# Performance work log

Hardware: AMD Instinct MI355X
Metric: run time of the kernel (lower is better)

Reference implementation:

```python
import jax, jax.numpy as jnp
import numpy as np
from jax import lax

B, S = 32, 256
V, D = 32000, 300   # pretrained word embeddings
P, PD = 35, 32      # pos vocab / pos embed dim (from source)
M = 66              # morph feature dim
H = 6               # LSTM units per direction -> bilstm_output_size = 12
A = 12


def _lstm(x, Wx, Wh, b, reverse=False):
    # x: [B,S,F] -> h: [B,S,H]; keras gate order i,f,c,o
    xg = x @ Wx + b  # precompute input projection once: [B,S,4H]
    def step(carry, xt):
        h, c = carry
        g = xt + h @ Wh
        i, f, cand, o = jnp.split(g, 4, axis=-1)
        c = jax.nn.sigmoid(f) * c + jax.nn.sigmoid(i) * jnp.tanh(cand)
        h = jax.nn.sigmoid(o) * jnp.tanh(c)
        return (h, c), h
    h0 = jnp.zeros((x.shape[0], Wh.shape[0]), x.dtype)
    _, hs = lax.scan(step, (h0, h0), jnp.swapaxes(xg, 0, 1), reverse=reverse)
    return jnp.swapaxes(hs, 0, 1)


def setup_inputs() -> dict:
    key = jax.random.key(0)
    ks = jax.random.split(key, 16)
    F = D + PD + M
    n = lambda k, shp, s=0.1: jax.random.normal(k, shp, dtype=jnp.float32) * s
    return {
        'words': jax.random.randint(ks[0], (B, S), 0, V),
        'pos': jax.random.randint(ks[1], (B, S), 0, P),
        'morph': jax.random.uniform(ks[2], (B, S, M), dtype=jnp.float32),
        'heads': jax.random.randint(ks[3], (B, S), 0, S),
        'word_table': n(ks[4], (V, D)),
        'pos_table': n(ks[5], (P, PD)),
        'Wx_f': n(ks[6], (F, 4 * H)), 'Wh_f': n(ks[7], (H, 4 * H)), 'b_f': jnp.zeros((4 * H,), jnp.float32),
        'Wx_b': n(ks[8], (F, 4 * H)), 'Wh_b': n(ks[9], (H, 4 * H)), 'b_b': jnp.zeros((4 * H,), jnp.float32),
        'Wu': n(ks[10], (A, A)), 'bu': jnp.zeros((A,), jnp.float32),
        'Ww': n(ks[11], (A, A)), 'bw': jnp.zeros((A,), jnp.float32),
        'v': n(ks[12], (A,)),
    }


def reference(words, pos, morph, heads, word_table, pos_table,
              Wx_f, Wh_f, b_f, Wx_b, Wh_b, b_b, Wu, bu, Ww, bw, v):
    # embed + concat -> [B,S,F]
    feats = jnp.concatenate([word_table[words], pos_table[pos], morph], axis=-1)
    # BiLSTM encoder -> [B,S,12] (dropout disabled / eval)
    hf = _lstm(feats, Wx_f, Wh_f, b_f)
    hb = _lstm(feats, Wx_b, Wh_b, b_b, reverse=True)
    repr_ = jnp.concatenate([hf, hb], axis=-1)
    # Bahdanau arc scoring, vectorized over dependant i (the tf loop):
    # scores[b,i,j] = v . tanh(u_a(repr)[b,j] + w_a(repr)[b,i])
    ua = repr_ @ Wu + bu  # head-position term (j)
    wa = repr_ @ Ww + bw  # dependant term (i)
    scores = jnp.einsum('bijd,d->bij', jnp.tanh(ua[:, None, :, :] + wa[:, :, None, :]), v)
    # the equality-based mask in tf picks out j == i (self cannot be head)
    eye = jnp.eye(S, dtype=bool)
    scores = jnp.where(eye[None], -10000.0, scores)
    # per-step sparse CE (from_logits, mean over batch), summed over i=1..S-1
    logp = jax.nn.log_softmax(scores, axis=-1)
    ce = -jnp.take_along_axis(logp, heads[:, :, None], axis=2)[..., 0]  # [B,S]
    loss = jnp.sum(jnp.mean(ce[:, 1:], axis=0))
    # parent_prob_table: exp(scores) concatenated along axis 0, i-major as in tf loop
    table = jnp.swapaxes(jnp.exp(scores[:, 1:, :]), 0, 1).reshape((S - 1) * B, S)
    return loss, table
```

## Files before the change

kernel.cpp:

```cpp
#include <hip/hip_runtime.h>
#include <hip/hip_bf16.h>

#define BB 32
#define SS 256
#define DD 300
#define PDD 32
#define MM 66
#define FF 398
#define HH 6
#define G4 24
#define AA 12
#define L2E 1.4426950408889634f

__device__ __forceinline__ float fast_rcp(float x) { return __builtin_amdgcn_rcpf(x); }
__device__ __forceinline__ float fast_tanh(float x) {
    return 1.f - 2.f * fast_rcp(__expf(2.f * x) + 1.f);
}
__device__ __forceinline__ float bcast_lane(float x, int l) {
    return __int_as_float(__builtin_amdgcn_readlane(__float_as_int(x), l));
}
template<int CTRL>
__device__ __forceinline__ float quad_bcast(float v) {
    return __int_as_float(__builtin_amdgcn_mov_dpp(__float_as_int(v), CTRL, 0xf, 0xf, true));
}

#define EPB 32
__global__ __launch_bounds__(256) void k_embed_proj(
    const int* __restrict__ words, const int* __restrict__ pos,
    const float* __restrict__ morph, const float* __restrict__ wtab,
    const float* __restrict__ ptab,
    const float* __restrict__ Wxf, const float* __restrict__ bfv,
    const float* __restrict__ Wxb, const float* __restrict__ bbv,
    float* __restrict__ xgf, float* __restrict__ xgb)
{
    __shared__ float4 sF[100][33];
    __shared__ float4 sW[48 * 100];
    int t  = threadIdx.x;
    int p0 = blockIdx.x * EPB;

    for (int idx = t; idx < EPB * 75; idx += 256) {
        int p = idx / 75, q = idx % 75;
        sF[q][p] = *(const float4*)(wtab + (size_t)words[p0 + p] * DD + 4 * q);
    }
    {
        int idx = t;
        int p = idx / 8, q = idx % 8;
        sF[75 + q][p] = *(const float4*)(ptab + pos[p0 + p] * PDD + 4 * q);
    }
    for (int idx = t; idx < EPB * 17; idx += 256) {
        int p = idx / 17, mq = idx % 17;
        const float2* ms = (const float2*)(morph + (size_t)(p0 + p) * MM);
        float2 lo = ms[2 * mq];
        float2 hi = (mq < 16) ? ms[2 * mq + 1] : make_float2(0.f, 0.f);
        sF[83 + mq][p] = make_float4(lo.x, lo.y, hi.x, hi.y);
    }
    {
        float* sWf = (float*)sW;
        for (int idx = t; idx < FF * G4; idx += 256) {
            int k = idx / G4, j = idx % G4;
            sWf[j * 400 + k]        = Wxf[idx];
            sWf[(24 + j) * 400 + k] = Wxb[idx];
        }
        if (t < 2 * G4) {
            int j = t >> 1, k = 398 + (t & 1);
            sWf[j * 400 + k] = 0.f; sWf[(24 + j) * 400 + k] = 0.f;
        }
    }
    __syncthreads();

    int lane = t & 63, w = t >> 6;
    int p    = lane & 31;
    int cg   = w * 2 + (lane >> 5);
    int dir  = cg >> 2;
    int tg   = cg & 3;
    int j0   = tg * 6;
    const float4* wc = sW + (dir * 24 + j0) * 100;

    float a0 = 0.f, a1 = 0.f, a2 = 0.f, a3 = 0.f, a4 = 0.f, a5 = 0.f;
    #pragma unroll 4
    for (int q = 0; q < 100; ++q) {
        float4 f = sF[q][p];
        float4 w0 = wc[0 * 100 + q], w1 = wc[1 * 100 + q], w2 = wc[2 * 100 + q];
        float4 w3 = wc[3 * 100 + q], w4 = wc[4 * 100 + q], w5 = wc[5 * 100 + q];
        a0 = fmaf(f.x, w0.x, a0); a0 = fmaf(f.y, w0.y, a0);
        a0 = fmaf(f.z, w0.z, a0); a0 = fmaf(f.w, w0.w, a0);
        a1 = fmaf(f.x, w1.x, a1); a1 = fmaf(f.y, w1.y, a1);
        a1 = fmaf(f.z, w1.z, a1); a1 = fmaf(f.w, w1.w, a1);
        a2 = fmaf(f.x, w2.x, a2); a2 = fmaf(f.y, w2.y, a2);
        a2 = fmaf(f.z, w2.z, a2); a2 = fmaf(f.w, w2.w, a2);
        a3 = fmaf(f.x, w3.x, a3); a3 = fmaf(f.y, w3.y, a3);
        a3 = fmaf(f.z, w3.z, a3); a3 = fmaf(f.w, w3.w, a3);
        a4 = fmaf(f.x, w4.x, a4); a4 = fmaf(f.y, w4.y, a4);
        a4 = fmaf(f.z, w4.z, a4); a4 = fmaf(f.w, w4.w, a4);
        a5 = fmaf(f.x, w5.x, a5); a5 = fmaf(f.y, w5.y, a5);
        a5 = fmaf(f.z, w5.z, a5); a5 = fmaf(f.w, w5.w, a5);
    }

    float kk = (tg == 2) ? 2.f * L2E : -L2E;
    const float* bias = dir ? bbv : bfv;
    float* o = (dir ? xgb : xgf) + (size_t)(p0 + p) * G4 + j0;
    o[0] = (a0 + bias[j0 + 0]) * kk; o[1] = (a1 + bias[j0 + 1]) * kk;
    o[2] = (a2 + bias[j0 + 2]) * kk; o[3] = (a3 + bias[j0 + 3]) * kk;
    o[4] = (a4 + bias[j0 + 4]) * kk; o[5] = (a5 + bias[j0 + 5]) * kk;
}

__global__ __launch_bounds__(64) void k_lstm(
    const float* __restrict__ xgf, const float* __restrict__ xgb,
    const float* __restrict__ Whf, const float* __restrict__ Whb,
    float* __restrict__ repr)
{
    __shared__ float sxg[(SS + 8) * G4];
    __shared__ float hbuf[SS * HH];
    int blk = blockIdx.x;
    int dir = blk >> 5;
    int b   = blk & 31;
    int lane = threadIdx.x;

    const float* xg = (dir ? xgb : xgf) + (size_t)b * SS * G4;
    const float* Wh = dir ? Whb : Whf;

    {
        const float4* src = (const float4*)xg;
        float4* dst = (float4*)sxg;
        #pragma unroll
        for (int u = 0; u < 24; ++u) {
            int d = lane + u * 64;
            int row = d / 6, c4 = d - row * 6;
            int drow = dir ? (SS - 1 - row) : row;
            dst[drow * 6 + c4] = src[d];
        }
        for (int g2 = lane; g2 < 8 * G4; g2 += 64) sxg[SS * G4 + g2] = 0.f;
    }

    int g    = lane % G4;
    int cell = g >> 2;
    int type = g & 3;
    int j    = type * HH + cell;

    float kk = (type == 2) ? 2.f * L2E : -L2E;
    float wh[HH];
    #pragma unroll
    for (int m = 0; m < HH; ++m) wh[m] = Wh[m * G4 + j] * kk;
    float Bc = (type == 2) ? 1.f : 0.f;
    float Ac = (type == 2) ? -1.f : 1.f;

    float sh[HH];
    #pragma unroll
    for (int m = 0; m < HH; ++m) sh[m] = 0.f;
    float c = 0.f;
    bool wr = (lane < G4) && ((lane & 3) == 0);
    __syncthreads();

    const float* xb = sxg + j;

    float pg[4];
    #pragma unroll
    for (int sl = 0; sl < 4; ++sl) pg[sl] = xb[sl * G4];

    #pragma unroll 1
    for (int t = 0; t < SS; t += 4) {
        #pragma unroll
        for (int sl = 0; sl < 4; ++sl) {
            float x = pg[sl];
            pg[sl] = xb[(t + 4 + sl) * G4];

            float aa  = fmaf(sh[1], wh[1], fmaf(sh[0], wh[0], x));
            float bb2 = fmaf(sh[3], wh[3], sh[2] * wh[2]);
            float cc2 = fmaf(sh[5], wh[5], sh[4] * wh[4]);
            x = (aa + bb2) + cc2;

            float e   = __builtin_amdgcn_exp2f(x);
            float val = fmaf(Bc, e, Ac) * fast_rcp(1.f + e);

            float vi = quad_bcast<0>(val);
            float vf = quad_bcast<85>(val);
            float vc = quad_bcast<170>(val);
            float vo = quad_bcast<255>(val);

            c = fmaf(vf, c, vi * vc);
            float ec = __builtin_amdgcn_exp2f(c * (2.f * L2E));
            float h  = (ec - 1.f) * fast_rcp(ec + 1.f) * vo;

            if (wr) hbuf[(t + sl) * HH + cell] = h;
            #pragma unroll
            for (int m = 0; m < HH; ++m) sh[m] = bcast_lane(h, 4 * m);
        }
    }
    __syncthreads();

    #pragma unroll
    for (int u = 0; u < (SS * HH) / 64; ++u) {
        int idx = lane + u * 64;
        int tt = idx / 6, cc = idx - tt * 6;
        int s = dir ? (SS - 1 - tt) : tt;
        repr[((size_t)b * SS + s) * (2 * HH) + dir * HH + cc] = hbuf[idx];
    }
}

__global__ __launch_bounds__(256) void k_uawa(
    const float* __restrict__ repr,
    const float* __restrict__ Wu, const float* __restrict__ bu,
    const float* __restrict__ Ww, const float* __restrict__ bw,
    float* __restrict__ ua, float* __restrict__ wa)
{
    int bs = blockIdx.x * blockDim.x + threadIdx.x;
    float r[AA];
    #pragma unroll
    for (int e = 0; e < AA; ++e) r[e] = repr[(size_t)bs * AA + e];
    #pragma unroll
    for (int d = 0; d < AA; ++d) {
        float au = bu[d], aw = bw[d];
        #pragma unroll
        for (int e = 0; e < AA; ++e) {
            au = fmaf(r[e], Wu[e * AA + d], au);
            aw = fmaf(r[e], Ww[e * AA + d], aw);
        }
        ua[(size_t)bs * AA + d] = au;
        wa[(size_t)bs * AA + d] = aw;
    }
}

__global__ __launch_bounds__(256) void k_score(
    const float* __restrict__ ua, const float* __restrict__ wa,
    const float* __restrict__ v, const int* __restrict__ heads,
    float* __restrict__ out, float* __restrict__ ce)
{
    int bi = blockIdx.x;
    int i  = bi & 255;
    int j  = threadIdx.x;

    __shared__ float swa[AA], sv[AA];
    if (j < AA) { swa[j] = wa[(size_t)bi * AA + j]; sv[j] = v[j]; }
    __syncthreads();

    const float* uj = ua + ((size_t)(bi & ~255) + j) * AA;
    float s = 0.f;
    #pragma unroll
    for (int d = 0; d < AA; ++d) s = fmaf(sv[d], fast_tanh(uj[d] + swa[d]), s);
    if (j == i) s = -10000.f;

    float e = __expf(s);
    if (i >= 1)
        out[1 + (((size_t)(i - 1) * BB + (bi >> 8)) * SS + j)] = e;

    float r = e;
    #pragma unroll
    for (int off = 32; off > 0; off >>= 1) r += __shfl_xor(r, off, 64);
    __shared__ float part[4];
    if ((j & 63) == 0) part[j >> 6] = r;
    __syncthreads();
    float tot = part[0] + part[1] + part[2] + part[3];

    if (j == heads[bi])
        ce[bi] = (i >= 1) ? (__logf(tot) - s) : 0.f;
}

__global__ __launch_bounds__(256) void k_loss(const float* __restrict__ ce,
                                              float* __restrict__ out)
{
    __shared__ float red[256];
    int t = threadIdx.x;
    float a = 0.f;
    for (int k = t; k < BB * SS; k += 256) a += ce[k];
    red[t] = a; __syncthreads();
    for (int off = 128; off > 0; off >>= 1) {
        if (t < off) red[t] += red[t + off];
        __syncthreads();
    }
    if (t == 0) out[0] = red[0] * (1.f / BB);
}

extern "C" void kernel_launch(void* const* d_in, const int* in_sizes, int n_in,
                              void* d_out, int out_size, void* d_ws, size_t ws_size,
                              hipStream_t stream)
{
    const int*   words = (const int*)  d_in[0];
    const int*   pos   = (const int*)  d_in[1];
    const float* morph = (const float*)d_in[2];
    const int*   heads = (const int*)  d_in[3];
    const float* wtab  = (const float*)d_in[4];
    const float* ptab  = (const float*)d_in[5];
    const float* Wxf   = (const float*)d_in[6];
    const float* Whf   = (const float*)d_in[7];
    const float* bf    = (const float*)d_in[8];
    const float* Wxb   = (const float*)d_in[9];
    const float* Whb   = (const float*)d_in[10];
    const float* bb    = (const float*)d_in[11];
    const float* Wu    = (const float*)d_in[12];
    const float* bu    = (const float*)d_in[13];
    const float* Ww    = (const float*)d_in[14];
    const float* bw    = (const float*)d_in[15];
    const float* v     = (const float*)d_in[16];
    float* out = (float*)d_out;

    float* xgf   = (float*)d_ws;
    float* xgb   = xgf   + (size_t)BB*SS*G4;
    float* repr  = xgb   + (size_t)BB*SS*G4;
    float* ua    = repr  + (size_t)BB*SS*2*HH;
    float* wa    = ua    + (size_t)BB*SS*AA;
    float* ce    = wa    + (size_t)BB*SS*AA;

    k_embed_proj<<<(BB * SS) / EPB, 256, 0, stream>>>(words, pos, morph, wtab, ptab,
                                                      Wxf, bf, Wxb, bb, xgf, xgb);
    k_lstm<<<BB * 2, 64, 0, stream>>>(xgf, xgb, Whf, Whb, repr);
    k_uawa<<<(BB * SS) / 256, 256, 0, stream>>>(repr, Wu, bu, Ww, bw, ua, wa);
    k_score<<<BB * SS, 256, 0, stream>>>(ua, wa, v, heads, out, ce);
    k_loss<<<1, 256, 0, stream>>>(ce, out);
}
```

Baseline: 73.80 us.

## Fuse LSTM recurrence with ua/wa projection in one block per batch

Merges the BiLSTM kernel and the ua/wa projection kernel. Each block now handles one batch element with two wavefronts, one per direction, and keeps both hidden-state sequences in shared memory. The projection is then computed directly from shared memory, so the repr buffer round trip and one kernel launch go away. In exchange the block count halves from 64 to 32 and each block needs more shared memory. The two directions now share a block, and the barrier before the recurrence is removed, which relies on each wave only reading its own staged data.

```diff
diff --git a/kernel.cpp b/kernel.cpp
--- a/kernel.cpp
+++ b/kernel.cpp
@@ -104,24 +104,25 @@
     o[4] = (a4 + bias[j0 + 4]) * kk; o[5] = (a5 + bias[j0 + 5]) * kk;
 }
 
-__global__ __launch_bounds__(64) void k_lstm(
+__global__ __launch_bounds__(128) void k_lstm_uawa(
     const float* __restrict__ xgf, const float* __restrict__ xgb,
     const float* __restrict__ Whf, const float* __restrict__ Whb,
-    float* __restrict__ repr)
-{
-    __shared__ float sxg[(SS + 8) * G4];
-    __shared__ float hbuf[SS * HH];
-    int blk = blockIdx.x;
-    int dir = blk >> 5;
-    int b   = blk & 31;
-    int lane = threadIdx.x;
+    const float* __restrict__ Wu, const float* __restrict__ bu,
+    const float* __restrict__ Ww, const float* __restrict__ bw,
+    float* __restrict__ ua, float* __restrict__ wa)
+{
+    __shared__ float sxg[2][(SS + 8) * G4];
+    __shared__ float hbuf[2][SS * HH];
+    int b    = blockIdx.x;
+    int lane = threadIdx.x & 63;
+    int dir  = __builtin_amdgcn_readfirstlane(threadIdx.x >> 6);
 
     const float* xg = (dir ? xgb : xgf) + (size_t)b * SS * G4;
     const float* Wh = dir ? Whb : Whf;
 
     {
         const float4* src = (const float4*)xg;
-        float4* dst = (float4*)sxg;
+        float4* dst = (float4*)sxg[dir];
         #pragma unroll
         for (int u = 0; u < 24; ++u) {
             int d = lane + u * 64;
@@ -129,7 +130,7 @@
             int drow = dir ? (SS - 1 - row) : row;
             dst[drow * 6 + c4] = src[d];
         }
-        for (int g2 = lane; g2 < 8 * G4; g2 += 64) sxg[SS * G4 + g2] = 0.f;
+        for (int g2 = lane; g2 < 8 * G4; g2 += 64) sxg[dir][SS * G4 + g2] = 0.f;
     }
 
     int g    = lane % G4;
@@ -149,9 +150,9 @@
     for (int m = 0; m < HH; ++m) sh[m] = 0.f;
     float c = 0.f;
     bool wr = (lane < G4) && ((lane & 3) == 0);
-    __syncthreads();
-
-    const float* xb = sxg + j;
+
+    const float* xb = sxg[dir] + j;
+    float* hb = hbuf[dir];
 
     float pg[4];
     #pragma unroll
@@ -181,7 +182,7 @@
             float ec = __builtin_amdgcn_exp2f(c * (2.f * L2E));
             float h  = (ec - 1.f) * fast_rcp(ec + 1.f) * vo;
 
-            if (wr) hbuf[(t + sl) * HH + cell] = h;
+            if (wr) hb[(t + sl) * HH + cell] = h;
             #pragma unroll
             for (int m = 0; m < HH; ++m) sh[m] = bcast_lane(h, 4 * m);
         }
@@ -189,34 +190,32 @@
     __syncthreads();
 
     #pragma unroll
-    for (int u = 0; u < (SS * HH) / 64; ++u) {
-        int idx = lane + u * 64;
-        int tt = idx / 6, cc = idx - tt * 6;
-        int s = dir ? (SS - 1 - tt) : tt;
-        repr[((size_t)b * SS + s) * (2 * HH) + dir * HH + cc] = hbuf[idx];
-    }
-}
-
-__global__ __launch_bounds__(256) void k_uawa(
-    const float* __restrict__ repr,
-    const float* __restrict__ Wu, const float* __restrict__ bu,
-    const float* __restrict__ Ww, const float* __restrict__ bw,
-    float* __restrict__ ua, float* __restrict__ wa)
-{
-    int bs = blockIdx.x * blockDim.x + threadIdx.x;
-    float r[AA];
-    #pragma unroll
-    for (int e = 0; e < AA; ++e) r[e] = repr[(size_t)bs * AA + e];
-    #pragma unroll
-    for (int d = 0; d < AA; ++d) {
-        float au = bu[d], aw = bw[d];
-        #pragma unroll
-        for (int e = 0; e < AA; ++e) {
-            au = fmaf(r[e], Wu[e * AA + d], au);
-            aw = fmaf(r[e], Ww[e * AA + d], aw);
-        }
-        ua[(size_t)bs * AA + d] = au;
-        wa[(size_t)bs * AA + d] = aw;
+    for (int half = 0; half < 2; ++half) {
+        int s = (int)threadIdx.x + half * 128;
+        float r[AA];
+        #pragma unroll
+        for (int cc = 0; cc < HH; ++cc) {
+            r[cc]      = hbuf[0][s * HH + cc];
+            r[HH + cc] = hbuf[1][(SS - 1 - s) * HH + cc];
+        }
+        float au[AA], aw[AA];
+        #pragma unroll
+        for (int d = 0; d < AA; ++d) { au[d] = bu[d]; aw[d] = bw[d]; }
+        #pragma unroll
+        for (int e2 = 0; e2 < AA; ++e2) {
+            #pragma unroll
+            for (int d = 0; d < AA; ++d) {
+                au[d] = fmaf(r[e2], Wu[e2 * AA + d], au[d]);
+                aw[d] = fmaf(r[e2], Ww[e2 * AA + d], aw[d]);
+            }
+        }
+        float* ou = ua + ((size_t)b * SS + s) * AA;
+        float* ow = wa + ((size_t)b * SS + s) * AA;
+        #pragma unroll
+        for (int d4 = 0; d4 < 3; ++d4) {
+            *(float4*)(ou + 4 * d4) = make_float4(au[4*d4], au[4*d4+1], au[4*d4+2], au[4*d4+3]);
+            *(float4*)(ow + 4 * d4) = make_float4(aw[4*d4], aw[4*d4+1], aw[4*d4+2], aw[4*d4+3]);
+        }
     }
 }
 
@@ -293,17 +292,15 @@
     const float* v     = (const float*)d_in[16];
     float* out = (float*)d_out;
 
-    float* xgf   = (float*)d_ws;
-    float* xgb   = xgf   + (size_t)BB*SS*G4;
-    float* repr  = xgb   + (size_t)BB*SS*G4;
-    float* ua    = repr  + (size_t)BB*SS*2*HH;
-    float* wa    = ua    + (size_t)BB*SS*AA;
-    float* ce    = wa    + (size_t)BB*SS*AA;
+    float* xgf  = (float*)d_ws;
+    float* xgb  = xgf  + (size_t)BB*SS*G4;
+    float* ua   = xgb  + (size_t)BB*SS*G4;
+    float* wa   = ua   + (size_t)BB*SS*AA;
+    float* ce   = wa   + (size_t)BB*SS*AA;
 
     k_embed_proj<<<(BB * SS) / EPB, 256, 0, stream>>>(words, pos, morph, wtab, ptab,
                                                       Wxf, bf, Wxb, bb, xgf, xgb);
-    k_lstm<<<BB * 2, 64, 0, stream>>>(xgf, xgb, Whf, Whb, repr);
-    k_uawa<<<(BB * SS) / 256, 256, 0, stream>>>(repr, Wu, bu, Ww, bw, ua, wa);
+    k_lstm_uawa<<<BB, 128, 0, stream>>>(xgf, xgb, Whf, Whb, Wu, bu, Ww, bw, ua, wa);
     k_score<<<BB * SS, 256, 0, stream>>>(ua, wa, v, heads, out, ce);
     k_loss<<<1, 256, 0, stream>>>(ce, out);
 }
```

Result: no change. 74.15 us (+0.5%).
